# Kernel optimization log

Measured on AMD Instinct MI355X. Metric: run time of the kernel, lower is better.

The kernel has to match this reference:

```python
import jax, jax.numpy as jnp
import numpy as np

B, T, E, D, A, H, C, K = 32, 1500, 512, 512, 512, 4, 10, 201
SHARPENING = 1.0


def setup_inputs() -> dict:
    key = jax.random.key(0)
    ks = jax.random.split(key, 11)
    def w(k, shape, fan_in):
        return jax.random.normal(k, shape, jnp.float32) / np.sqrt(fan_in).astype(np.float32)
    return {
        "enc_out": jax.random.normal(ks[0], (B, T, E), jnp.float32),
        "x_lens": jax.random.randint(ks[1], (B,), T // 2, T + 1),
        "dec_out": jax.random.normal(ks[2], (B, 1, D), jnp.float32),
        # previous-step attention weights: a valid distribution over T per head
        "aw_step": jax.nn.softmax(jax.random.normal(ks[3], (B, T, H), jnp.float32), axis=1),
        "w_enc": w(ks[4], (H, E, A), E),   # per-head LinearND(enc->att)
        "b_enc": jnp.zeros((H, A), jnp.float32),
        "w_dec": w(ks[5], (H, D, A), D),   # per-head LinearND(dec->att), no bias
        "w_conv": w(ks[6], (H, C, A), C),  # per-head LinearND(conv_ch->att), no bias
        "conv_k": w(ks[7], (H * C, 1, K), K),  # grouped 1D conv kernels (O,I,K), groups=H
        "v": w(ks[8], (H, A), A),          # per-head LinearND(att->1), no bias
        "w_mha": w(ks[9], (H * E, E), H * E),
        "b_mha": jnp.zeros((E,), jnp.float32),
    }


def reference(enc_out, x_lens, dec_out, aw_step, w_enc, b_enc, w_dec, w_conv, conv_k, v, w_mha, b_mha):
    b, t, e = enc_out.shape
    h = aw_step.shape[-1]
    c = w_conv.shape[1]
    k = conv_k.shape[-1]
    # enc_out_a: per-head encoder projection [B,T,H,A]
    enc_a = jnp.einsum('bte,hea->btha', enc_out, w_enc) + b_enc
    # decoder projection, broadcast over time [B,1,H,A]
    dec_a = jnp.einsum('bd,hda->bha', dec_out[:, 0], w_dec)[:, None]
    # location features: grouped 1D conv over previous attention weights
    aw_t = jnp.transpose(aw_step, (0, 2, 1))  # [B,H,T]
    conv = jax.lax.conv_general_dilated(
        aw_t, conv_k, window_strides=(1,), padding=[(k // 2, k // 2)],
        dimension_numbers=('NCH', 'OIH', 'NCH'), feature_group_count=h)  # [B,H*C,T]
    conv = conv.reshape(b, h, c, t).transpose(0, 3, 1, 2)  # [B,T,H,C]
    conv_a = jnp.einsum('bthc,hca->btha', conv, w_conv)
    # additive energy [B,T,H]
    energy = jnp.einsum('btha,ha->bth', jnp.tanh(enc_a + dec_a + conv_a), v)
    # original code multiplies energy by mask (1 valid, -1024 padded) then sharpening
    mask = jnp.where(jnp.arange(t)[None, :] < x_lens[:, None], 1.0, -1024.0).astype(energy.dtype)
    energy = energy * mask[:, :, None] * SHARPENING
    aw = jax.nn.softmax(energy, axis=1)  # softmax over time per head
    # per-head context, concatenated along feature dim -> [B,1,H*E]
    ctx = jnp.einsum('bte,bth->bhe', enc_out, aw).reshape(b, 1, h * e)
    ctx = ctx @ w_mha + b_mha  # [B,1,E]
    return ctx, aw
```

## Files before the change

kernel.cpp:

```cpp
#include <hip/hip_runtime.h>
#include <hip/hip_bf16.h>

#define BB 32
#define TT 1500
#define TP 1536
#define EE 512
#define HH 4
#define AA 512
#define NN 2048
#define CC 10
#define KCONV 201
#define KAUG 576

typedef __attribute__((ext_vector_type(8))) __bf16 bf16x8;
typedef __attribute__((ext_vector_type(4))) float f32x4;

__device__ __forceinline__ unsigned short f2bf(float x) {
    unsigned int u = __float_as_uint(x);
    u = (u + 0x7fffu + ((u >> 16) & 1u)) >> 16;
    return (unsigned short)u;
}
__device__ __forceinline__ float bf2f(unsigned short u) {
    return __uint_as_float(((unsigned int)u) << 16);
}
__device__ __forceinline__ void glds16(const void* g, void* l) {
    __builtin_amdgcn_global_load_lds(
        (const __attribute__((address_space(1))) unsigned int*)g,
        (__attribute__((address_space(3))) unsigned int*)l, 16, 0, 0);
}
__device__ __forceinline__ float tanh_fast(float x) {
    float e = __expf(x * 2.0f);
    return fmaf(-2.0f, __builtin_amdgcn_rcpf(e + 1.0f), 1.0f);
}
__device__ __forceinline__ unsigned int pkbf(float x, float y) {
    float2 f{x, y};
    __hip_bfloat162 h2 = __float22bfloat162_rn(f);
    return *reinterpret_cast<unsigned int*>(&h2);
}
__device__ __forceinline__ void split2(float x, float y, unsigned int& h, unsigned int& l) {
    unsigned short hx = f2bf(x), hy = f2bf(y);
    h = ((unsigned int)hy << 16) | hx;
    l = pkbf(x - bf2f(hx), y - bf2f(hy));
}

#define PREP_ZERO0  0
#define PREP_DEC0   1024
#define PREP_CONV0  2048
#define PREP_WT0    9728
#define PREP_TOTAL  10016

__global__ __launch_bounds__(256) void k_prep(
    const float* __restrict__ dec_out, const float* __restrict__ aw_step,
    const float* __restrict__ w_enc, const float* __restrict__ b_enc,
    const float* __restrict__ w_dec, const float* __restrict__ w_conv,
    const float* __restrict__ conv_k,
    unsigned short* __restrict__ Whi, unsigned short* __restrict__ Wlo,
    unsigned short* __restrict__ Chi, unsigned short* __restrict__ Clo,
    float* __restrict__ dec_a, float* __restrict__ zbase) {
    __shared__ float sh[64 * 65];
    const int bid = blockIdx.x;
    const int tid = threadIdx.x;

    if (bid < PREP_DEC0) {
        zbase[bid * 256 + tid] = 0.f;
    } else if (bid < PREP_CONV0) {
        const int rb = bid - PREP_DEC0;
        const int b  = rb >> 5;
        const int n0 = (rb & 31) * 64;
        const int n  = n0 + (tid & 63);
        const int dg = tid >> 6;
        const int h  = n >> 9, a = n & 511;
        const float* dp = dec_out + (size_t)b * 512 + dg * 128;
        const float* wp = w_dec + ((size_t)h * 512 + dg * 128) * 512 + a;
        float acc = 0.f;
#pragma unroll 8
        for (int d = 0; d < 128; ++d) acc += dp[d] * wp[(size_t)d * 512];
        sh[tid] = acc;
        __syncthreads();
        if (tid < 64) {
            float tot = sh[tid] + sh[tid + 64] + sh[tid + 128] + sh[tid + 192];
            dec_a[(size_t)b * NN + n0 + tid] = b_enc[n0 + tid] + tot;
        }
    } else if (bid < PREP_WT0) {
        int r = bid - PREP_CONV0;
        const int tch = r % 6;
        const int hc  = (r / 6) % 40;
        const int b   = r / 240;
        const int h   = hc / 10;
        const int t0  = tch * 256;
        float* sAw = sh;
        for (int i = tid; i < 456; i += 256) {
            int ts = t0 - 100 + i;
            sAw[i] = (ts >= 0 && ts < TT) ? aw_step[((size_t)b * TT + ts) * HH + h] : 0.f;
        }
        __syncthreads();
        int t = t0 + tid;
        if (t < TT) {
            const float* ck = conv_k + (size_t)hc * KCONV;
            float acc = 0.f;
#pragma unroll 4
            for (int k = 0; k < KCONV; ++k) acc += sAw[tid + k] * ck[k];
            size_t o = ((size_t)b * TP + t) * 64 + hc;
            unsigned short hi = f2bf(acc);
            Chi[o] = hi; Clo[o] = f2bf(acc - bf2f(hi));
        }
    } else {
        int r = bid - PREP_WT0;
        const int h  = r / 72;
        const int rr = r % 72;
        const int at = rr / 9;
        const int kt = rr % 9;
        const int a0 = at * 64;
        if (kt < 8) {
            const int k0 = kt * 64;
#pragma unroll
            for (int it = 0; it < 16; ++it) {
                int kk = it * 4 + (tid >> 6);
                int aa = tid & 63;
                sh[kk * 65 + aa] = w_enc[((size_t)h * 512 + k0 + kk) * 512 + a0 + aa];
            }
            __syncthreads();
#pragma unroll
            for (int it = 0; it < 16; ++it) {
                int nl = it * 4 + (tid >> 6);
                int kk = tid & 63;
                float val = sh[kk * 65 + nl];
                size_t o = ((size_t)h * 512 + a0 + nl) * KAUG + k0 + kk;
                unsigned short hi = f2bf(val);
                Whi[o] = hi; Wlo[o] = f2bf(val - bf2f(hi));
            }
        } else {
#pragma unroll
            for (int it = 0; it < 16; ++it) {
                int nl = it * 4 + (tid >> 6);
                int j  = tid & 63;
                float val = 0.f;
                if (j < 40 && (j / 10) == h)
                    val = w_conv[((size_t)h * 10 + (j % 10)) * 512 + a0 + nl];
                size_t o = ((size_t)h * 512 + a0 + nl) * KAUG + 512 + j;
                unsigned short hi = f2bf(val);
                Whi[o] = hi; Wlo[o] = f2bf(val - bf2f(hi));
            }
        }
    }
}

__global__ __launch_bounds__(256) void k_gemm(
    const float* __restrict__ enc,
    const unsigned short* __restrict__ Chi, const unsigned short* __restrict__ Clo,
    const unsigned short* __restrict__ Whi, const unsigned short* __restrict__ Wlo,
    const float* __restrict__ dec_a, const float* __restrict__ vvec,
    const int* __restrict__ xl, float* __restrict__ energy) {
    __shared__ unsigned short lsAhi[4096], lsAlo[4096];
    __shared__ unsigned short lsBhi[4096], lsBlo[4096];
    const int id = blockIdx.x;
    const int xcd = id & 7;
    const int s = id >> 3;
    const int ntile = s & 15;
    const int tile = (s >> 4) * 8 + xcd;
    const int mtile = 11 - (tile >> 5);
    const int b = tile & 31;
    const int tid = threadIdx.x;
    const int lane = tid & 63, wave = tid >> 6;
    const int wm = wave >> 1, wn = wave & 1;
    const int m0 = mtile * 128, n0 = ntile * 128;
    const int xlen = xl[b];

    f32x4 acc[4][4];
#pragma unroll
    for (int i = 0; i < 4; i++)
#pragma unroll
        for (int j = 0; j < 4; j++) acc[i][j] = (f32x4){0.f, 0.f, 0.f, 0.f};

    const int row = tid >> 2;
    const int ko  = (tid & 3) * 8;
    const size_t bbase = ((size_t)n0 + row) * KAUG + ko;
    const size_t cbase = ((size_t)b * TP + m0 + row) * 64 + ko;
    const int l1 = tid * 8;
    const int l2 = l1 + 2048;
    const int ar = wm * 64, br = wn * 64;
    const int fo = (lane & 15) * 32 + (lane >> 4) * 8;

    const float* ap0 = enc + ((size_t)b * TT + m0 + row) * 512 + ko;
    const float* ap1 = ap0 + (size_t)64 * 512;

    if (m0 + 128 <= xlen) {
        float4 fa0 = *(const float4*)(ap0);
        float4 fa1 = *(const float4*)(ap0 + 4);
        float4 fa2 = *(const float4*)(ap1);
        float4 fa3 = *(const float4*)(ap1 + 4);
        for (int ks = 0; ks < 18; ++ks) {
            const int k0 = ks * 32;
            __syncthreads();
            glds16(Whi + bbase + k0,                     &lsBhi[l1]);
            glds16(Whi + bbase + k0 + (size_t)64 * KAUG, &lsBhi[l2]);
            if (ks < 16) {
                uint4 w0, w1;
                w0.x = pkbf(fa0.x, fa0.y); w0.y = pkbf(fa0.z, fa0.w);
                w0.z = pkbf(fa1.x, fa1.y); w0.w = pkbf(fa1.z, fa1.w);
                w1.x = pkbf(fa2.x, fa2.y); w1.y = pkbf(fa2.z, fa2.w);
                w1.z = pkbf(fa3.x, fa3.y); w1.w = pkbf(fa3.z, fa3.w);
                *reinterpret_cast<uint4*>(&lsAhi[l1]) = w0;
                *reinterpret_cast<uint4*>(&lsAhi[l2]) = w1;
            } else {
                glds16(Chi + cbase + (ks - 16) * 32,        &lsAhi[l1]);
                glds16(Chi + cbase + (ks - 16) * 32 + 4096, &lsAhi[l2]);
            }
            asm volatile("s_waitcnt vmcnt(0)" ::: "memory");
            __syncthreads();

            bf16x8 ah[4], bh[4];
#pragma unroll
            for (int i = 0; i < 4; i++) {
                ah[i] = *(const bf16x8*)&lsAhi[(ar + i * 16) * 32 + fo];
                bh[i] = *(const bf16x8*)&lsBhi[(br + i * 16) * 32 + fo];
            }
            if (ks < 15) {
                const int nk = k0 + 32;
                fa0 = *(const float4*)(ap0 + nk);
                fa1 = *(const float4*)(ap0 + nk + 4);
                fa2 = *(const float4*)(ap1 + nk);
                fa3 = *(const float4*)(ap1 + nk + 4);
            }
#pragma unroll
            for (int i = 0; i < 4; i++)
#pragma unroll
                for (int j = 0; j < 4; j++)
                    acc[i][j] = __builtin_amdgcn_mfma_f32_16x16x32_bf16(ah[i], bh[j], acc[i][j], 0, 0, 0);
        }
    } else {
        const bool g1 = (m0 + row + 64) < TT;
        const float4 z4 = {0.f, 0.f, 0.f, 0.f};
        bool corr[4];
#pragma unroll
        for (int i = 0; i < 4; i++) corr[i] = (m0 + ar + i * 16 + 16) > xlen;
        float4 fa0 = *(const float4*)(ap0);
        float4 fa1 = *(const float4*)(ap0 + 4);
        float4 fa2 = g1 ? *(const float4*)(ap1) : z4;
        float4 fa3 = g1 ? *(const float4*)(ap1 + 4) : z4;
        for (int ks = 0; ks < 18; ++ks) {
            const int k0 = ks * 32;
            __syncthreads();
            glds16(Whi + bbase + k0,                     &lsBhi[l1]);
            glds16(Whi + bbase + k0 + (size_t)64 * KAUG, &lsBhi[l2]);
            glds16(Wlo + bbase + k0,                     &lsBlo[l1]);
            glds16(Wlo + bbase + k0 + (size_t)64 * KAUG, &lsBlo[l2]);
            if (ks < 16) {
                uint4 h0, h1, e0, e1;
                split2(fa0.x, fa0.y, h0.x, e0.x); split2(fa0.z, fa0.w, h0.y, e0.y);
                split2(fa1.x, fa1.y, h0.z, e0.z); split2(fa1.z, fa1.w, h0.w, e0.w);
                split2(fa2.x, fa2.y, h1.x, e1.x); split2(fa2.z, fa2.w, h1.y, e1.y);
                split2(fa3.x, fa3.y, h1.z, e1.z); split2(fa3.z, fa3.w, h1.w, e1.w);
                *reinterpret_cast<uint4*>(&lsAhi[l1]) = h0;
                *reinterpret_cast<uint4*>(&lsAhi[l2]) = h1;
                *reinterpret_cast<uint4*>(&lsAlo[l1]) = e0;
                *reinterpret_cast<uint4*>(&lsAlo[l2]) = e1;
            } else {
                glds16(Chi + cbase + (ks - 16) * 32,        &lsAhi[l1]);
                glds16(Chi + cbase + (ks - 16) * 32 + 4096, &lsAhi[l2]);
                glds16(Clo + cbase + (ks - 16) * 32,        &lsAlo[l1]);
                glds16(Clo + cbase + (ks - 16) * 32 + 4096, &lsAlo[l2]);
            }
            asm volatile("s_waitcnt vmcnt(0)" ::: "memory");
            __syncthreads();

            bf16x8 ah[4], al[4], bh[4], bl[4];
#pragma unroll
            for (int i = 0; i < 4; i++) {
                ah[i] = *(const bf16x8*)&lsAhi[(ar + i * 16) * 32 + fo];
                al[i] = *(const bf16x8*)&lsAlo[(ar + i * 16) * 32 + fo];
                bh[i] = *(const bf16x8*)&lsBhi[(br + i * 16) * 32 + fo];
                bl[i] = *(const bf16x8*)&lsBlo[(br + i * 16) * 32 + fo];
            }
            if (ks < 15) {
                const int nk = k0 + 32;
                fa0 = *(const float4*)(ap0 + nk);
                fa1 = *(const float4*)(ap0 + nk + 4);
                fa2 = g1 ? *(const float4*)(ap1 + nk) : z4;
                fa3 = g1 ? *(const float4*)(ap1 + nk + 4) : z4;
            }
#pragma unroll
            for (int i = 0; i < 4; i++) {
#pragma unroll
                for (int j = 0; j < 4; j++)
                    acc[i][j] = __builtin_amdgcn_mfma_f32_16x16x32_bf16(ah[i], bh[j], acc[i][j], 0, 0, 0);
                if (corr[i]) {
#pragma unroll
                    for (int j = 0; j < 4; j++) {
                        acc[i][j] = __builtin_amdgcn_mfma_f32_16x16x32_bf16(ah[i], bl[j], acc[i][j], 0, 0, 0);
                        acc[i][j] = __builtin_amdgcn_mfma_f32_16x16x32_bf16(al[i], bh[j], acc[i][j], 0, 0, 0);
                    }
                }
            }
        }
    }

    const int h = ntile >> 2;
    const int kg = lane >> 4;
    float dv[4], vv[4];
#pragma unroll
    for (int j = 0; j < 4; j++) {
        int ng = n0 + wn * 64 + j * 16 + (lane & 15);
        dv[j] = dec_a[(size_t)b * NN + ng];
        vv[j] = vvec[ng];
    }
#pragma unroll
    for (int i = 0; i < 4; i++) {
        float part[4] = {0.f, 0.f, 0.f, 0.f};
#pragma unroll
        for (int j = 0; j < 4; j++)
#pragma unroll
            for (int r = 0; r < 4; r++)
                part[r] += tanh_fast(acc[i][j][r] + dv[j]) * vv[j];
#pragma unroll
        for (int r = 0; r < 4; r++) {
            float s = part[r];
            s += __shfl_xor(s, 1, 64);
            s += __shfl_xor(s, 2, 64);
            s += __shfl_xor(s, 4, 64);
            s += __shfl_xor(s, 8, 64);
            if ((lane & 15) == 0) {
                int t = m0 + wm * 64 + i * 16 + kg * 4 + r;
                if (t < TT)
                    atomicAdd(&energy[((size_t)b * HH + h) * TP + t], s);
            }
        }
    }
}

__global__ __launch_bounds__(1024) void k_softmax(const float* __restrict__ energy,
                                                  const int* __restrict__ x_lens,
                                                  float* __restrict__ aw) {
    const int b = blockIdx.x >> 2, h = blockIdx.x & 3;
    const int tid = threadIdx.x;
    __shared__ float sE[TT];
    __shared__ float red[1024];
    const int xlen = x_lens[b];
    float lmax = -3.4e38f;
    for (int t = tid; t < TT; t += 1024) {
        float e = energy[((size_t)b * HH + h) * TP + t];
        float m = (t < xlen) ? e : e * -1024.0f;
        sE[t] = m;
        lmax = fmaxf(lmax, m);
    }
    red[tid] = lmax; __syncthreads();
    for (int s = 512; s > 0; s >>= 1) { if (tid < s) red[tid] = fmaxf(red[tid], red[tid + s]); __syncthreads(); }
    float mx = red[0]; __syncthreads();
    float lsum = 0.f;
    for (int t = tid; t < TT; t += 1024) {
        float ex = __expf(sE[t] - mx);
        sE[t] = ex; lsum += ex;
    }
    red[tid] = lsum; __syncthreads();
    for (int s = 512; s > 0; s >>= 1) { if (tid < s) red[tid] += red[tid + s]; __syncthreads(); }
    float rs = 1.0f / red[0];
    for (int t = tid; t < TT; t += 1024)
        aw[((size_t)b * TT + t) * HH + h] = sE[t] * rs;
}

__global__ __launch_bounds__(256) void k_ctx(const float* __restrict__ enc,
                                             const float* __restrict__ aw,
                                             float* __restrict__ ctx_h) {
    const int chunk = blockIdx.x, b = blockIdx.y;
    const int t0 = chunk * 64;
    const int nt = (TT - t0 < 64) ? (TT - t0) : 64;
    __shared__ float sA[64 * 4];
    __shared__ float4 red4[128][4];
    __shared__ int s_nz;
    const int tid = threadIdx.x;
    if (tid == 0) s_nz = 0;
    __syncthreads();
    for (int i = tid; i < nt * 4; i += 256) {
        float w = aw[((size_t)b * TT + t0) * HH + i];
        sA[i] = w;
        if (w != 0.f) s_nz = 1;
    }
    __syncthreads();
    if (!s_nz) return;
    const int e4 = (tid & 127) * 4;
    const int tg = tid >> 7;
    const float* ep = enc + ((size_t)b * TT + t0) * EE + e4;
    float acc[4][4] = {};
#pragma unroll 4
    for (int tt = tg; tt < nt; tt += 2) {
        float4 ev = *reinterpret_cast<const float4*>(ep + (size_t)tt * EE);
        float w0 = sA[tt * 4 + 0], w1 = sA[tt * 4 + 1];
        float w2 = sA[tt * 4 + 2], w3 = sA[tt * 4 + 3];
        acc[0][0] += w0 * ev.x; acc[0][1] += w0 * ev.y; acc[0][2] += w0 * ev.z; acc[0][3] += w0 * ev.w;
        acc[1][0] += w1 * ev.x; acc[1][1] += w1 * ev.y; acc[1][2] += w1 * ev.z; acc[1][3] += w1 * ev.w;
        acc[2][0] += w2 * ev.x; acc[2][1] += w2 * ev.y; acc[2][2] += w2 * ev.z; acc[2][3] += w2 * ev.w;
        acc[3][0] += w3 * ev.x; acc[3][1] += w3 * ev.y; acc[3][2] += w3 * ev.z; acc[3][3] += w3 * ev.w;
    }
    if (tg == 1) {
#pragma unroll
        for (int h = 0; h < 4; ++h)
            red4[tid & 127][h] = make_float4(acc[h][0], acc[h][1], acc[h][2], acc[h][3]);
    }
    __syncthreads();
    if (tg == 0) {
#pragma unroll
        for (int h = 0; h < 4; ++h) {
            float4 o = red4[tid][h];
            float* dst = &ctx_h[((size_t)b * HH + h) * EE + e4];
            atomicAdd(dst + 0, acc[h][0] + o.x);
            atomicAdd(dst + 1, acc[h][1] + o.y);
            atomicAdd(dst + 2, acc[h][2] + o.z);
            atomicAdd(dst + 3, acc[h][3] + o.w);
        }
    }
}

__global__ __launch_bounds__(256) void k_mha(const float* __restrict__ ctx_h,
                                             const float* __restrict__ w_mha,
                                             const float* __restrict__ b_mha,
                                             float* __restrict__ out) {
    __shared__ float sred[256];
    const int tid = threadIdx.x;
    const int b  = blockIdx.x >> 2;
    const int eo = ((blockIdx.x & 3) << 7) + (tid & 127);
    const int kg = tid >> 7;
    const float* c = ctx_h + (size_t)b * NN + kg * 1024;
    const float* w = w_mha + ((size_t)kg * 1024) * EE + eo;
    float acc = 0.f;
#pragma unroll 8
    for (int k = 0; k < 1024; ++k) acc += c[k] * w[(size_t)k * EE];
    sred[tid] = acc;
    __syncthreads();
    if (tid < 128)
        out[(size_t)b * EE + eo] = b_mha[eo] + sred[tid] + sred[tid + 128];
}

extern "C" void kernel_launch(void* const* d_in, const int* in_sizes, int n_in,
                              void* d_out, int out_size, void* d_ws, size_t ws_size,
                              hipStream_t stream) {
    (void)in_sizes; (void)n_in; (void)out_size;
    const float* enc    = (const float*)d_in[0];
    const int*   xlen   = (const int*)d_in[1];
    const float* dec    = (const float*)d_in[2];
    const float* aw_in  = (const float*)d_in[3];
    const float* w_enc  = (const float*)d_in[4];
    const float* b_enc  = (const float*)d_in[5];
    const float* w_dec  = (const float*)d_in[6];
    const float* w_conv = (const float*)d_in[7];
    const float* convk  = (const float*)d_in[8];
    const float* v      = (const float*)d_in[9];
    const float* w_mha  = (const float*)d_in[10];
    const float* b_mha  = (const float*)d_in[11];
    float* out = (float*)d_out;

    char* ws = (char*)d_ws;
    unsigned short* Whi = (unsigned short*)ws;
    unsigned short* Wlo = (unsigned short*)(ws + 2359296);
    unsigned short* Chi = (unsigned short*)(ws + 4718592);
    unsigned short* Clo = (unsigned short*)(ws + 11010048);
    float* dec_a  = (float*)(ws + 17301504);
    float* energy = (float*)(ws + 17563648);
    float* ctx_h  = (float*)(ws + 18350080);
    (void)ws_size;

    k_prep<<<dim3(PREP_TOTAL), 256, 0, stream>>>(dec, aw_in, w_enc, b_enc,
                                                 w_dec, w_conv, convk,
                                                 Whi, Wlo, Chi, Clo, dec_a, energy);
    k_gemm<<<dim3(6144), 256, 0, stream>>>(enc, Chi, Clo, Whi, Wlo, dec_a, v, xlen, energy);
    k_softmax<<<dim3(BB * HH), 1024, 0, stream>>>(energy, xlen, out + 16384);
    k_ctx <<<dim3(24, BB), 256, 0, stream>>>(enc, out + 16384, ctx_h);
    k_mha <<<dim3(128), 256, 0, stream>>>(ctx_h, w_mha, b_mha, out);
}
```

Measured before the change: 714.1 us.

## Split GEMM into valid/padded kernels and load MFMA operands directly from global

Replaces the single LDS-staged GEMM with two kernels, one for fully valid time tiles (bf16 only) and one for tiles that touch padding (split hi/lo correction). Each lane now loads its MFMA fragments straight from global memory into registers, dropping LDS staging and the block barriers. The XCD-aware block swizzle is replaced by a plain 3D grid with early exit. Operand reuse across waves through LDS is lost, so global/L2 traffic per block rises, and half the launched blocks in each kernel exit immediately.

After: 0.9998 ms. 40.0% more time.

```diff
diff --git a/kernel.cpp b/kernel.cpp
--- a/kernel.cpp
+++ b/kernel.cpp
@@ -15,6 +15,8 @@
 typedef __attribute__((ext_vector_type(8))) __bf16 bf16x8;
 typedef __attribute__((ext_vector_type(4))) float f32x4;
 
+union U16 { uint4 u; bf16x8 v; };
+
 __device__ __forceinline__ unsigned short f2bf(float x) {
     unsigned int u = __float_as_uint(x);
     u = (u + 0x7fffu + ((u >> 16) & 1u)) >> 16;
@@ -22,11 +24,6 @@
 }
 __device__ __forceinline__ float bf2f(unsigned short u) {
     return __uint_as_float(((unsigned int)u) << 16);
-}
-__device__ __forceinline__ void glds16(const void* g, void* l) {
-    __builtin_amdgcn_global_load_lds(
-        (const __attribute__((address_space(1))) unsigned int*)g,
-        (__attribute__((address_space(3))) unsigned int*)l, 16, 0, 0);
 }
 __device__ __forceinline__ float tanh_fast(float x) {
     float e = __expf(x * 2.0f);
@@ -145,157 +142,10 @@
     }
 }
 
-__global__ __launch_bounds__(256) void k_gemm(
-    const float* __restrict__ enc,
-    const unsigned short* __restrict__ Chi, const unsigned short* __restrict__ Clo,
-    const unsigned short* __restrict__ Whi, const unsigned short* __restrict__ Wlo,
-    const float* __restrict__ dec_a, const float* __restrict__ vvec,
-    const int* __restrict__ xl, float* __restrict__ energy) {
-    __shared__ unsigned short lsAhi[4096], lsAlo[4096];
-    __shared__ unsigned short lsBhi[4096], lsBlo[4096];
-    const int id = blockIdx.x;
-    const int xcd = id & 7;
-    const int s = id >> 3;
-    const int ntile = s & 15;
-    const int tile = (s >> 4) * 8 + xcd;
-    const int mtile = 11 - (tile >> 5);
-    const int b = tile & 31;
-    const int tid = threadIdx.x;
-    const int lane = tid & 63, wave = tid >> 6;
-    const int wm = wave >> 1, wn = wave & 1;
-    const int m0 = mtile * 128, n0 = ntile * 128;
-    const int xlen = xl[b];
-
-    f32x4 acc[4][4];
-#pragma unroll
-    for (int i = 0; i < 4; i++)
-#pragma unroll
-        for (int j = 0; j < 4; j++) acc[i][j] = (f32x4){0.f, 0.f, 0.f, 0.f};
-
-    const int row = tid >> 2;
-    const int ko  = (tid & 3) * 8;
-    const size_t bbase = ((size_t)n0 + row) * KAUG + ko;
-    const size_t cbase = ((size_t)b * TP + m0 + row) * 64 + ko;
-    const int l1 = tid * 8;
-    const int l2 = l1 + 2048;
-    const int ar = wm * 64, br = wn * 64;
-    const int fo = (lane & 15) * 32 + (lane >> 4) * 8;
-
-    const float* ap0 = enc + ((size_t)b * TT + m0 + row) * 512 + ko;
-    const float* ap1 = ap0 + (size_t)64 * 512;
-
-    if (m0 + 128 <= xlen) {
-        float4 fa0 = *(const float4*)(ap0);
-        float4 fa1 = *(const float4*)(ap0 + 4);
-        float4 fa2 = *(const float4*)(ap1);
-        float4 fa3 = *(const float4*)(ap1 + 4);
-        for (int ks = 0; ks < 18; ++ks) {
-            const int k0 = ks * 32;
-            __syncthreads();
-            glds16(Whi + bbase + k0,                     &lsBhi[l1]);
-            glds16(Whi + bbase + k0 + (size_t)64 * KAUG, &lsBhi[l2]);
-            if (ks < 16) {
-                uint4 w0, w1;
-                w0.x = pkbf(fa0.x, fa0.y); w0.y = pkbf(fa0.z, fa0.w);
-                w0.z = pkbf(fa1.x, fa1.y); w0.w = pkbf(fa1.z, fa1.w);
-                w1.x = pkbf(fa2.x, fa2.y); w1.y = pkbf(fa2.z, fa2.w);
-                w1.z = pkbf(fa3.x, fa3.y); w1.w = pkbf(fa3.z, fa3.w);
-                *reinterpret_cast<uint4*>(&lsAhi[l1]) = w0;
-                *reinterpret_cast<uint4*>(&lsAhi[l2]) = w1;
-            } else {
-                glds16(Chi + cbase + (ks - 16) * 32,        &lsAhi[l1]);
-                glds16(Chi + cbase + (ks - 16) * 32 + 4096, &lsAhi[l2]);
-            }
-            asm volatile("s_waitcnt vmcnt(0)" ::: "memory");
-            __syncthreads();
-
-            bf16x8 ah[4], bh[4];
-#pragma unroll
-            for (int i = 0; i < 4; i++) {
-                ah[i] = *(const bf16x8*)&lsAhi[(ar + i * 16) * 32 + fo];
-                bh[i] = *(const bf16x8*)&lsBhi[(br + i * 16) * 32 + fo];
-            }
-            if (ks < 15) {
-                const int nk = k0 + 32;
-                fa0 = *(const float4*)(ap0 + nk);
-                fa1 = *(const float4*)(ap0 + nk + 4);
-                fa2 = *(const float4*)(ap1 + nk);
-                fa3 = *(const float4*)(ap1 + nk + 4);
-            }
-#pragma unroll
-            for (int i = 0; i < 4; i++)
-#pragma unroll
-                for (int j = 0; j < 4; j++)
-                    acc[i][j] = __builtin_amdgcn_mfma_f32_16x16x32_bf16(ah[i], bh[j], acc[i][j], 0, 0, 0);
-        }
-    } else {
-        const bool g1 = (m0 + row + 64) < TT;
-        const float4 z4 = {0.f, 0.f, 0.f, 0.f};
-        bool corr[4];
-#pragma unroll
-        for (int i = 0; i < 4; i++) corr[i] = (m0 + ar + i * 16 + 16) > xlen;
-        float4 fa0 = *(const float4*)(ap0);
-        float4 fa1 = *(const float4*)(ap0 + 4);
-        float4 fa2 = g1 ? *(const float4*)(ap1) : z4;
-        float4 fa3 = g1 ? *(const float4*)(ap1 + 4) : z4;
-        for (int ks = 0; ks < 18; ++ks) {
-            const int k0 = ks * 32;
-            __syncthreads();
-            glds16(Whi + bbase + k0,                     &lsBhi[l1]);
-            glds16(Whi + bbase + k0 + (size_t)64 * KAUG, &lsBhi[l2]);
-            glds16(Wlo + bbase + k0,                     &lsBlo[l1]);
-            glds16(Wlo + bbase + k0 + (size_t)64 * KAUG, &lsBlo[l2]);
-            if (ks < 16) {
-                uint4 h0, h1, e0, e1;
-                split2(fa0.x, fa0.y, h0.x, e0.x); split2(fa0.z, fa0.w, h0.y, e0.y);
-                split2(fa1.x, fa1.y, h0.z, e0.z); split2(fa1.z, fa1.w, h0.w, e0.w);
-                split2(fa2.x, fa2.y, h1.x, e1.x); split2(fa2.z, fa2.w, h1.y, e1.y);
-                split2(fa3.x, fa3.y, h1.z, e1.z); split2(fa3.z, fa3.w, h1.w, e1.w);
-                *reinterpret_cast<uint4*>(&lsAhi[l1]) = h0;
-                *reinterpret_cast<uint4*>(&lsAhi[l2]) = h1;
-                *reinterpret_cast<uint4*>(&lsAlo[l1]) = e0;
-                *reinterpret_cast<uint4*>(&lsAlo[l2]) = e1;
-            } else {
-                glds16(Chi + cbase + (ks - 16) * 32,        &lsAhi[l1]);
-                glds16(Chi + cbase + (ks - 16) * 32 + 4096, &lsAhi[l2]);
-                glds16(Clo + cbase + (ks - 16) * 32,        &lsAlo[l1]);
-                glds16(Clo + cbase + (ks - 16) * 32 + 4096, &lsAlo[l2]);
-            }
-            asm volatile("s_waitcnt vmcnt(0)" ::: "memory");
-            __syncthreads();
-
-            bf16x8 ah[4], al[4], bh[4], bl[4];
-#pragma unroll
-            for (int i = 0; i < 4; i++) {
-                ah[i] = *(const bf16x8*)&lsAhi[(ar + i * 16) * 32 + fo];
-                al[i] = *(const bf16x8*)&lsAlo[(ar + i * 16) * 32 + fo];
-                bh[i] = *(const bf16x8*)&lsBhi[(br + i * 16) * 32 + fo];
-                bl[i] = *(const bf16x8*)&lsBlo[(br + i * 16) * 32 + fo];
-            }
-            if (ks < 15) {
-                const int nk = k0 + 32;
-                fa0 = *(const float4*)(ap0 + nk);
-                fa1 = *(const float4*)(ap0 + nk + 4);
-                fa2 = g1 ? *(const float4*)(ap1 + nk) : z4;
-                fa3 = g1 ? *(const float4*)(ap1 + nk + 4) : z4;
-            }
-#pragma unroll
-            for (int i = 0; i < 4; i++) {
-#pragma unroll
-                for (int j = 0; j < 4; j++)
-                    acc[i][j] = __builtin_amdgcn_mfma_f32_16x16x32_bf16(ah[i], bh[j], acc[i][j], 0, 0, 0);
-                if (corr[i]) {
-#pragma unroll
-                    for (int j = 0; j < 4; j++) {
-                        acc[i][j] = __builtin_amdgcn_mfma_f32_16x16x32_bf16(ah[i], bl[j], acc[i][j], 0, 0, 0);
-                        acc[i][j] = __builtin_amdgcn_mfma_f32_16x16x32_bf16(al[i], bh[j], acc[i][j], 0, 0, 0);
-                    }
-                }
-            }
-        }
-    }
-
-    const int h = ntile >> 2;
+__device__ __forceinline__ void gemm_epilogue(
+    f32x4 (&acc)[4][4], const float* __restrict__ dec_a, const float* __restrict__ vvec,
+    float* __restrict__ energy, int b, int m0, int n0, int wm, int wn, int lane) {
+    const int h = n0 >> 9;
     const int kg = lane >> 4;
     float dv[4], vv[4];
 #pragma unroll
@@ -326,6 +176,168 @@
             }
         }
     }
+}
+
+__global__ __launch_bounds__(256) void k_gemm_v(
+    const float* __restrict__ enc, const unsigned short* __restrict__ Chi,
+    const unsigned short* __restrict__ Whi,
+    const float* __restrict__ dec_a, const float* __restrict__ vvec,
+    const int* __restrict__ xl, float* __restrict__ energy) {
+    const int ntile = blockIdx.x, mtile = blockIdx.y, b = blockIdx.z;
+    const int m0 = mtile * 128, n0 = ntile * 128;
+    if (m0 + 128 > xl[b]) return;
+    const int tid = threadIdx.x;
+    const int lane = tid & 63, wave = tid >> 6;
+    const int wm = wave >> 1, wn = wave & 1;
+    const int ar = wm * 64, br = wn * 64;
+    const int mrow = lane & 15;
+    const int kq = (lane >> 4) * 8;
+
+    f32x4 acc[4][4];
+#pragma unroll
+    for (int i = 0; i < 4; i++)
+#pragma unroll
+        for (int j = 0; j < 4; j++) acc[i][j] = (f32x4){0.f, 0.f, 0.f, 0.f};
+
+    const float* ap[4];
+    const unsigned short* bp[4];
+#pragma unroll
+    for (int i = 0; i < 4; i++) {
+        ap[i] = enc + ((size_t)b * TT + m0 + ar + i * 16 + mrow) * 512 + kq;
+        bp[i] = Whi + ((size_t)(n0 + br + i * 16 + mrow)) * KAUG + kq;
+    }
+
+#pragma unroll 2
+    for (int ks = 0; ks < 16; ++ks) {
+        const int k0 = ks * 32;
+        U16 av[4], bv[4];
+#pragma unroll
+        for (int i = 0; i < 4; i++) {
+            float4 f0 = *(const float4*)(ap[i] + k0);
+            float4 f1 = *(const float4*)(ap[i] + k0 + 4);
+            av[i].u.x = pkbf(f0.x, f0.y); av[i].u.y = pkbf(f0.z, f0.w);
+            av[i].u.z = pkbf(f1.x, f1.y); av[i].u.w = pkbf(f1.z, f1.w);
+            bv[i].u = *(const uint4*)(bp[i] + k0);
+        }
+#pragma unroll
+        for (int i = 0; i < 4; i++)
+#pragma unroll
+            for (int j = 0; j < 4; j++)
+                acc[i][j] = __builtin_amdgcn_mfma_f32_16x16x32_bf16(av[i].v, bv[j].v, acc[i][j], 0, 0, 0);
+    }
+#pragma unroll
+    for (int ks = 16; ks < 18; ++ks) {
+        U16 av[4], bv[4];
+#pragma unroll
+        for (int i = 0; i < 4; i++) {
+            av[i].u = *(const uint4*)(Chi + ((size_t)b * TP + m0 + ar + i * 16 + mrow) * 64 + (ks - 16) * 32 + kq);
+            bv[i].u = *(const uint4*)(bp[i] + ks * 32);
+        }
+#pragma unroll
+        for (int i = 0; i < 4; i++)
+#pragma unroll
+            for (int j = 0; j < 4; j++)
+                acc[i][j] = __builtin_amdgcn_mfma_f32_16x16x32_bf16(av[i].v, bv[j].v, acc[i][j], 0, 0, 0);
+    }
+
+    gemm_epilogue(acc, dec_a, vvec, energy, b, m0, n0, wm, wn, lane);
+}
+
+__global__ __launch_bounds__(256) void k_gemm_p(
+    const float* __restrict__ enc,
+    const unsigned short* __restrict__ Chi, const unsigned short* __restrict__ Clo,
+    const unsigned short* __restrict__ Whi, const unsigned short* __restrict__ Wlo,
+    const float* __restrict__ dec_a, const float* __restrict__ vvec,
+    const int* __restrict__ xl, float* __restrict__ energy) {
+    const int ntile = blockIdx.x, mtile = blockIdx.y, b = blockIdx.z;
+    const int m0 = mtile * 128, n0 = ntile * 128;
+    const int xlen = xl[b];
+    if (m0 + 128 <= xlen) return;
+    const int tid = threadIdx.x;
+    const int lane = tid & 63, wave = tid >> 6;
+    const int wm = wave >> 1, wn = wave & 1;
+    const int ar = wm * 64, br = wn * 64;
+    const int mrow = lane & 15;
+    const int kq = (lane >> 4) * 8;
+
+    f32x4 acc[4][4];
+#pragma unroll
+    for (int i = 0; i < 4; i++)
+#pragma unroll
+        for (int j = 0; j < 4; j++) acc[i][j] = (f32x4){0.f, 0.f, 0.f, 0.f};
+
+    bool corr[4];
+#pragma unroll
+    for (int i = 0; i < 4; i++) corr[i] = (m0 + ar + i * 16 + 16) > xlen;
+
+    const float* ap[4];
+    const unsigned short* bph[4];
+    const unsigned short* bpl[4];
+#pragma unroll
+    for (int i = 0; i < 4; i++) {
+        int t = m0 + ar + i * 16 + mrow;
+        int tc = t < TT ? t : TT - 1;
+        ap[i]  = enc + ((size_t)b * TT + tc) * 512 + kq;
+        bph[i] = Whi + ((size_t)(n0 + br + i * 16 + mrow)) * KAUG + kq;
+        bpl[i] = Wlo + ((size_t)(n0 + br + i * 16 + mrow)) * KAUG + kq;
+    }
+
+#pragma unroll 2
+    for (int ks = 0; ks < 16; ++ks) {
+        const int k0 = ks * 32;
+        U16 ah[4], al[4], bh[4], bl[4];
+#pragma unroll
+        for (int i = 0; i < 4; i++) {
+            float4 f0 = *(const float4*)(ap[i] + k0);
+            float4 f1 = *(const float4*)(ap[i] + k0 + 4);
+            split2(f0.x, f0.y, ah[i].u.x, al[i].u.x);
+            split2(f0.z, f0.w, ah[i].u.y, al[i].u.y);
+            split2(f1.x, f1.y, ah[i].u.z, al[i].u.z);
+            split2(f1.z, f1.w, ah[i].u.w, al[i].u.w);
+            bh[i].u = *(const uint4*)(bph[i] + k0);
+            bl[i].u = *(const uint4*)(bpl[i] + k0);
+        }
+#pragma unroll
+        for (int i = 0; i < 4; i++) {
+#pragma unroll
+            for (int j = 0; j < 4; j++)
+                acc[i][j] = __builtin_amdgcn_mfma_f32_16x16x32_bf16(ah[i].v, bh[j].v, acc[i][j], 0, 0, 0);
+            if (corr[i]) {
+#pragma unroll
+                for (int j = 0; j < 4; j++) {
+                    acc[i][j] = __builtin_amdgcn_mfma_f32_16x16x32_bf16(ah[i].v, bl[j].v, acc[i][j], 0, 0, 0);
+                    acc[i][j] = __builtin_amdgcn_mfma_f32_16x16x32_bf16(al[i].v, bh[j].v, acc[i][j], 0, 0, 0);
+                }
+            }
+        }
+    }
+#pragma unroll
+    for (int ks = 16; ks < 18; ++ks) {
+        U16 ah[4], al[4], bh[4], bl[4];
+#pragma unroll
+        for (int i = 0; i < 4; i++) {
+            size_t co = ((size_t)b * TP + m0 + ar + i * 16 + mrow) * 64 + (ks - 16) * 32 + kq;
+            ah[i].u = *(const uint4*)(Chi + co);
+            al[i].u = *(const uint4*)(Clo + co);
+            bh[i].u = *(const uint4*)(bph[i] + ks * 32);
+            bl[i].u = *(const uint4*)(bpl[i] + ks * 32);
+        }
+#pragma unroll
+        for (int i = 0; i < 4; i++) {
+#pragma unroll
+            for (int j = 0; j < 4; j++)
+                acc[i][j] = __builtin_amdgcn_mfma_f32_16x16x32_bf16(ah[i].v, bh[j].v, acc[i][j], 0, 0, 0);
+            if (corr[i]) {
+#pragma unroll
+                for (int j = 0; j < 4; j++) {
+                    acc[i][j] = __builtin_amdgcn_mfma_f32_16x16x32_bf16(ah[i].v, bl[j].v, acc[i][j], 0, 0, 0);
+                    acc[i][j] = __builtin_amdgcn_mfma_f32_16x16x32_bf16(al[i].v, bh[j].v, acc[i][j], 0, 0, 0);
+                }
+            }
+        }
+    }
+
+    gemm_epilogue(acc, dec_a, vvec, energy, b, m0, n0, wm, wn, lane);
 }
 
 __global__ __launch_bounds__(1024) void k_softmax(const float* __restrict__ energy,
@@ -461,7 +473,8 @@
     k_prep<<<dim3(PREP_TOTAL), 256, 0, stream>>>(dec, aw_in, w_enc, b_enc,
                                                  w_dec, w_conv, convk,
                                                  Whi, Wlo, Chi, Clo, dec_a, energy);
-    k_gemm<<<dim3(6144), 256, 0, stream>>>(enc, Chi, Clo, Whi, Wlo, dec_a, v, xlen, energy);
+    k_gemm_v<<<dim3(16, 12, BB), 256, 0, stream>>>(enc, Chi, Whi, dec_a, v, xlen, energy);
+    k_gemm_p<<<dim3(16, 12, BB), 256, 0, stream>>>(enc, Chi, Clo, Whi, Wlo, dec_a, v, xlen, energy);
     k_softmax<<<dim3(BB * HH), 1024, 0, stream>>>(energy, xlen, out + 16384);
     k_ctx <<<dim3(24, BB), 256, 0, stream>>>(enc, out + 16384, ctx_h);
     k_mha <<<dim3(128), 256, 0, stream>>>(ctx_h, w_mha, b_mha, out);
```
